# Kernel tuning notes

Hardware: AMD Instinct MI355X
Metric: run time of the kernel (lower is better)

Reference implementation:

```python
import jax, jax.numpy as jnp
import numpy as np

D_MODEL, D_FF, N_EXPERTS, TOP_K = 1024, 4096, 8, 2


def setup_inputs() -> dict:
    key = jax.random.key(0)
    k1, k2, k3, k4 = jax.random.split(key, 4)
    x = jax.random.normal(k1, (2, 2048, D_MODEL), dtype=jnp.float32)
    Wg = jax.random.normal(k2, (D_MODEL, N_EXPERTS), dtype=jnp.float32) * 0.02
    W1 = jax.random.normal(k3, (N_EXPERTS, D_MODEL, D_FF), dtype=jnp.float32) * 0.02
    b1 = jnp.zeros((N_EXPERTS, D_FF), dtype=jnp.float32)
    W2 = jax.random.normal(k4, (N_EXPERTS, D_FF, D_MODEL), dtype=jnp.float32) * 0.02
    b2 = jnp.zeros((N_EXPERTS, D_MODEL), dtype=jnp.float32)
    return {"x": x, "Wg": Wg, "W1": W1, "b1": b1, "W2": W2, "b2": b2}


def reference(x, Wg, W1, b1, W2, b2):
    B, S, D = x.shape
    T = B * S
    flat_x = x.reshape(T, D)                      # [T, D]
    # Router: softmax over expert logits, keep top-k experts per token.
    logits = flat_x @ Wg                          # [T, E]
    probs = jax.nn.softmax(logits, axis=-1)       # [T, E]
    _, top_idx = jax.lax.top_k(probs, TOP_K)      # [T, K]
    # mask[t, e] = 1 if expert e is among token t's top-k
    mask = jax.nn.one_hot(top_idx, N_EXPERTS, dtype=probs.dtype).sum(axis=1)  # [T, E]
    weights = probs * mask                        # gating score only for routed experts
    # Dense grouped expert MLP: every expert applied to all tokens, then masked-combined.
    h = jax.nn.gelu(jnp.einsum('td,edh->eth', flat_x, W1) + b1[:, None, :])  # [E, T, H]
    y = jnp.einsum('eth,ehd->etd', h, W2) + b2[:, None, :]                   # [E, T, D]
    out = jnp.einsum('etd,te->td', y, weights)                               # [T, D]
    return out.reshape(B, S, D)
```

## Files before the change

kernel.cpp:

```cpp
#include <hip/hip_runtime.h>
#include <hip/hip_bf16.h>

#define D_MODEL 1024
#define D_FF    4096
#define N_EXPERTS 8
#define TOPK    2
#define T_TOK   4096
#define NPAIR   (T_TOK * TOPK)
#define MT_MAX  32

typedef __attribute__((ext_vector_type(8))) short s8v;
typedef __attribute__((ext_vector_type(4))) float f4v;
typedef __attribute__((ext_vector_type(8))) unsigned short u16x8;

__device__ __forceinline__ void async16(const void* g, void* l) {
    __builtin_amdgcn_global_load_lds(
        (const __attribute__((address_space(1))) void*)g,
        (__attribute__((address_space(3))) void*)l, 16, 0, 0);
}

__device__ __forceinline__ float gelu_tanh(float v) {
    float u = 0.7978845608028654f * (v + 0.044715f * v * v * v);
    float t = 1.0f - 2.0f / (1.0f + __expf(2.0f * u));
    return 0.5f * v * (1.0f + t);
}

__device__ __forceinline__ unsigned short f2bf(float f) {
    union { __hip_bfloat16 b; unsigned short u; } cv;
    cv.b = __float2bfloat16(f);
    return cv.u;
}

__global__ __launch_bounds__(256) void router_kernel(
    const float* __restrict__ x, const float* __restrict__ Wg,
    int* __restrict__ top_e, float* __restrict__ top_w,
    int* __restrict__ counts)
{
    int wave = threadIdx.x >> 6;
    int lane = threadIdx.x & 63;
    int t = blockIdx.x * 4 + wave;
    if (t >= T_TOK) return;

    float acc[8] = {0.f,0.f,0.f,0.f,0.f,0.f,0.f,0.f};
    const float* xr = x + (size_t)t * D_MODEL;
    for (int d = lane; d < D_MODEL; d += 64) {
        float xv = xr[d];
        const float* wr = Wg + d * N_EXPERTS;
        float4 w0 = *(const float4*)wr;
        float4 w1 = *(const float4*)(wr + 4);
        acc[0] += xv * w0.x; acc[1] += xv * w0.y;
        acc[2] += xv * w0.z; acc[3] += xv * w0.w;
        acc[4] += xv * w1.x; acc[5] += xv * w1.y;
        acc[6] += xv * w1.z; acc[7] += xv * w1.w;
    }
    #pragma unroll
    for (int off = 32; off >= 1; off >>= 1) {
        #pragma unroll
        for (int e = 0; e < 8; e++) acc[e] += __shfl_xor(acc[e], off);
    }
    if (lane == 0) {
        float m = acc[0];
        #pragma unroll
        for (int e = 1; e < 8; e++) m = fmaxf(m, acc[e]);
        float p[8]; float s = 0.f;
        #pragma unroll
        for (int e = 0; e < 8; e++) { p[e] = expf(acc[e] - m); s += p[e]; }
        float inv = 1.f / s;
        #pragma unroll
        for (int e = 0; e < 8; e++) p[e] *= inv;
        int i0 = 0; float b0 = p[0];
        #pragma unroll
        for (int e = 1; e < 8; e++) if (p[e] > b0) { b0 = p[e]; i0 = e; }
        int i1 = -1; float b1 = -1.f;
        #pragma unroll
        for (int e = 0; e < 8; e++) if (e != i0 && p[e] > b1) { b1 = p[e]; i1 = e; }
        top_e[2*t]   = i0; top_w[2*t]   = b0;
        top_e[2*t+1] = i1; top_w[2*t+1] = b1;
        atomicAdd(&counts[i0], 1);
        atomicAdd(&counts[i1], 1);
    }
}

__global__ void offsets_kernel(const int* __restrict__ counts, int* __restrict__ offsets)
{
    if (threadIdx.x == 0 && blockIdx.x == 0) {
        int run = 0;
        for (int e = 0; e < N_EXPERTS; e++) { offsets[e] = run; run += counts[e]; }
        offsets[N_EXPERTS] = run;
    }
}

__global__ __launch_bounds__(256) void scatter_kernel(
    const int* __restrict__ top_e, const int* __restrict__ offsets,
    int* __restrict__ counts2, int* __restrict__ pair_id)
{
    int t = blockIdx.x * blockDim.x + threadIdx.x;
    if (t >= T_TOK) return;
    #pragma unroll
    for (int k = 0; k < TOPK; k++) {
        int e = top_e[2*t + k];
        int pos = atomicAdd(&counts2[e], 1);
        pair_id[offsets[e] + pos] = 2*t + k;
    }
}

__global__ __launch_bounds__(256) void cast_x_kernel(
    const float* __restrict__ x, __hip_bfloat16* __restrict__ xb)
{
    int i = (blockIdx.x * 256 + threadIdx.x) * 8;
    float4 a = *(const float4*)(x + i);
    float4 b = *(const float4*)(x + i + 4);
    unsigned short t[8];
    t[0]=f2bf(a.x); t[1]=f2bf(a.y); t[2]=f2bf(a.z); t[3]=f2bf(a.w);
    t[4]=f2bf(b.x); t[5]=f2bf(b.y); t[6]=f2bf(b.z); t[7]=f2bf(b.w);
    *(u16x8*)((unsigned short*)xb + i) = *(u16x8*)t;
}

__global__ __launch_bounds__(256) void transpose_cast_kernel(
    const float* __restrict__ src, __hip_bfloat16* __restrict__ dst, int R, int C)
{
    int e = blockIdx.z;
    src += (size_t)e * R * C;
    dst += (size_t)e * R * C;
    int b0 = blockIdx.x * 64;
    int a0 = blockIdx.y * 64;

    __shared__ float tile[64][65];
    int tid = threadIdx.x;
    int lr = tid >> 4;
    int lc = (tid & 15) * 4;
    #pragma unroll
    for (int rr = 0; rr < 4; rr++) {
        int r = lr + rr * 16;
        *(float4*)&tile[r][lc] = *(const float4*)(src + (size_t)(a0 + r) * C + b0 + lc);
    }
    __syncthreads();
    int oc = tid >> 3;
    int oj = (tid & 7) * 8;
    #pragma unroll
    for (int rr = 0; rr < 2; rr++) {
        int c = oc + rr * 32;
        unsigned short t[8];
        #pragma unroll
        for (int j = 0; j < 8; j++) t[j] = f2bf(tile[oj + j][c]);
        *(u16x8*)((unsigned short*)dst + (size_t)(b0 + c) * R + a0 + oj) = *(u16x8*)t;
    }
}

__global__ __launch_bounds__(256) void gemm1_mfma(
    const __hip_bfloat16* __restrict__ xb, const __hip_bfloat16* __restrict__ W1T,
    const float* __restrict__ b1,
    const int* __restrict__ offsets, const int* __restrict__ pair_id,
    __hip_bfloat16* __restrict__ h)
{
    int e  = blockIdx.y >> 5;
    int mt = blockIdx.y & 31;
    int off_e = offsets[e];
    int cnt   = offsets[e + 1] - off_e;
    int m0 = mt * 128;
    if (m0 >= cnt) return;
    int n0 = blockIdx.x * 128;

    __shared__ __hip_bfloat16 As[128 * 32];
    __shared__ __hip_bfloat16 Bs[128 * 32];
    __shared__ int pid[128];

    int tid = threadIdx.x;
    if (tid < 128) {
        int r = m0 + tid; if (r >= cnt) r = cnt - 1;
        pid[tid] = pair_id[off_e + r];
    }
    __syncthreads();

    int lane = tid & 63, wid = tid >> 6;
    int ia0 = wid * 64 + lane;
    int ia1 = ia0 + 256;
    int rA0 = ia0 >> 2, kA0 = (ia0 & 3) * 8;
    int rA1 = ia1 >> 2, kA1 = (ia1 & 3) * 8;

    const __hip_bfloat16* gA0 = xb + (size_t)(pid[rA0] >> 1) * D_MODEL + kA0;
    const __hip_bfloat16* gA1 = xb + (size_t)(pid[rA1] >> 1) * D_MODEL + kA1;
    const __hip_bfloat16* WT  = W1T + (size_t)e * (D_MODEL * D_FF);
    const __hip_bfloat16* gB0 = WT + (size_t)(n0 + rA0) * D_MODEL + kA0;
    const __hip_bfloat16* gB1 = WT + (size_t)(n0 + rA1) * D_MODEL + kA1;

    int fm = lane & 15;
    int fk = (lane >> 4) * 8;
    int wm = (wid >> 1) * 64;
    int wn = (wid & 1) * 64;

    f4v acc[4][4];
    #pragma unroll
    for (int i = 0; i < 4; i++)
        #pragma unroll
        for (int j = 0; j < 4; j++)
            acc[i][j] = (f4v){0.f, 0.f, 0.f, 0.f};

    for (int k0 = 0; k0 < D_MODEL; k0 += 32) {
        async16(gA0 + k0, As + ia0 * 8);
        async16(gA1 + k0, As + ia1 * 8);
        async16(gB0 + k0, Bs + ia0 * 8);
        async16(gB1 + k0, Bs + ia1 * 8);
        __syncthreads();
        s8v af[4], bfr[4];
        #pragma unroll
        for (int i = 0; i < 4; i++)
            af[i] = *(const s8v*)(As + (wm + i * 16 + fm) * 32 + fk);
        #pragma unroll
        for (int j = 0; j < 4; j++)
            bfr[j] = *(const s8v*)(Bs + (wn + j * 16 + fm) * 32 + fk);
        #pragma unroll
        for (int i = 0; i < 4; i++)
            #pragma unroll
            for (int j = 0; j < 4; j++)
                acc[i][j] = __builtin_amdgcn_mfma_f32_16x16x32_bf16(af[i], bfr[j], acc[i][j], 0, 0, 0);
        __syncthreads();
    }

    int rq = (lane >> 4) * 4;
    #pragma unroll
    for (int i = 0; i < 4; i++) {
        #pragma unroll
        for (int j = 0; j < 4; j++) {
            int n = n0 + wn + j * 16 + fm;
            float bias = b1[e * D_FF + n];
            #pragma unroll
            for (int r = 0; r < 4; r++) {
                int m = wm + i * 16 + rq + r;
                if (m0 + m < cnt) {
                    float v = acc[i][j][r] + bias;
                    h[(size_t)(off_e + m0 + m) * D_FF + n] = __float2bfloat16(gelu_tanh(v));
                }
            }
        }
    }
}

__global__ __launch_bounds__(256) void gemm2_mfma(
    const __hip_bfloat16* __restrict__ h, const __hip_bfloat16* __restrict__ W2T,
    const float* __restrict__ b2,
    const int* __restrict__ offsets, const int* __restrict__ pair_id,
    float* __restrict__ y)
{
    int e  = blockIdx.y >> 5;
    int mt = blockIdx.y & 31;
    int off_e = offsets[e];
    int cnt   = offsets[e + 1] - off_e;
    int m0 = mt * 128;
    if (m0 >= cnt) return;
    int n0 = blockIdx.x * 128;

    __shared__ __hip_bfloat16 As[128 * 32];
    __shared__ __hip_bfloat16 Bs[128 * 32];
    __shared__ int pid[128];

    int tid = threadIdx.x;
    if (tid < 128) {
        int r = m0 + tid; if (r >= cnt) r = cnt - 1;
        pid[tid] = pair_id[off_e + r];
    }
    __syncthreads();

    int lane = tid & 63, wid = tid >> 6;
    int ia0 = wid * 64 + lane;
    int ia1 = ia0 + 256;
    int rA0 = ia0 >> 2, kA0 = (ia0 & 3) * 8;
    int rA1 = ia1 >> 2, kA1 = (ia1 & 3) * 8;
    int mr0 = m0 + rA0; if (mr0 >= cnt) mr0 = cnt - 1;
    int mr1 = m0 + rA1; if (mr1 >= cnt) mr1 = cnt - 1;

    const __hip_bfloat16* gA0 = h + (size_t)(off_e + mr0) * D_FF + kA0;
    const __hip_bfloat16* gA1 = h + (size_t)(off_e + mr1) * D_FF + kA1;
    const __hip_bfloat16* WT  = W2T + (size_t)e * (D_FF * D_MODEL);
    const __hip_bfloat16* gB0 = WT + (size_t)(n0 + rA0) * D_FF + kA0;
    const __hip_bfloat16* gB1 = WT + (size_t)(n0 + rA1) * D_FF + kA1;

    int fm = lane & 15;
    int fk = (lane >> 4) * 8;
    int wm = (wid >> 1) * 64;
    int wn = (wid & 1) * 64;

    f4v acc[4][4];
    #pragma unroll
    for (int i = 0; i < 4; i++)
        #pragma unroll
        for (int j = 0; j < 4; j++)
            acc[i][j] = (f4v){0.f, 0.f, 0.f, 0.f};

    for (int k0 = 0; k0 < D_FF; k0 += 32) {
        async16(gA0 + k0, As + ia0 * 8);
        async16(gA1 + k0, As + ia1 * 8);
        async16(gB0 + k0, Bs + ia0 * 8);
        async16(gB1 + k0, Bs + ia1 * 8);
        __syncthreads();
        s8v af[4], bfr[4];
        #pragma unroll
        for (int i = 0; i < 4; i++)
            af[i] = *(const s8v*)(As + (wm + i * 16 + fm) * 32 + fk);
        #pragma unroll
        for (int j = 0; j < 4; j++)
            bfr[j] = *(const s8v*)(Bs + (wn + j * 16 + fm) * 32 + fk);
        #pragma unroll
        for (int i = 0; i < 4; i++)
            #pragma unroll
            for (int j = 0; j < 4; j++)
                acc[i][j] = __builtin_amdgcn_mfma_f32_16x16x32_bf16(af[i], bfr[j], acc[i][j], 0, 0, 0);
        __syncthreads();
    }

    int rq = (lane >> 4) * 4;
    #pragma unroll
    for (int i = 0; i < 4; i++) {
        #pragma unroll
        for (int j = 0; j < 4; j++) {
            int n = n0 + wn + j * 16 + fm;
            float bias = b2[e * D_MODEL + n];
            #pragma unroll
            for (int r = 0; r < 4; r++) {
                int m = wm + i * 16 + rq + r;
                if (m0 + m < cnt) {
                    int p = pid[m];
                    y[(size_t)p * D_MODEL + n] = acc[i][j][r] + bias;
                }
            }
        }
    }
}

__global__ __launch_bounds__(256) void combine_kernel(
    const float* __restrict__ y, const float* __restrict__ top_w,
    float* __restrict__ out)
{
    int gid = blockIdx.x * blockDim.x + threadIdx.x;
    int t = gid >> 8;
    int c = gid & 255;
    float w0 = top_w[2*t];
    float w1 = top_w[2*t + 1];
    const float4* y0 = (const float4*)(y + (size_t)(2*t) * D_MODEL);
    const float4* y1 = (const float4*)(y + (size_t)(2*t + 1) * D_MODEL);
    float4 a = y0[c], b = y1[c];
    float4 o;
    o.x = w0*a.x + w1*b.x; o.y = w0*a.y + w1*b.y;
    o.z = w0*a.z + w1*b.z; o.w = w0*a.w + w1*b.w;
    ((float4*)out)[gid] = o;
}

extern "C" void kernel_launch(void* const* d_in, const int* in_sizes, int n_in,
                              void* d_out, int out_size, void* d_ws, size_t ws_size,
                              hipStream_t stream)
{
    const float* x  = (const float*)d_in[0];
    const float* Wg = (const float*)d_in[1];
    const float* W1 = (const float*)d_in[2];
    const float* b1 = (const float*)d_in[3];
    const float* W2 = (const float*)d_in[4];
    const float* b2 = (const float*)d_in[5];
    float* out = (float*)d_out;

    char* ws = (char*)d_ws;
    size_t off = 0;
    int*   top_e   = (int*)(ws + off);  off += (size_t)NPAIR * 4;
    float* top_w   = (float*)(ws + off); off += (size_t)NPAIR * 4;
    int*   counts  = (int*)(ws + off);
    int*   counts2 = counts + N_EXPERTS;
    int*   offsets = counts2 + N_EXPERTS; off += 256;
    int*   pair_id = (int*)(ws + off);  off += (size_t)NPAIR * 4;
    off = (off + 255) & ~(size_t)255;
    __hip_bfloat16* xb  = (__hip_bfloat16*)(ws + off); off += (size_t)T_TOK * D_MODEL * 2;
    __hip_bfloat16* W1T = (__hip_bfloat16*)(ws + off); off += (size_t)N_EXPERTS * D_MODEL * D_FF * 2;
    __hip_bfloat16* W2T = (__hip_bfloat16*)(ws + off); off += (size_t)N_EXPERTS * D_MODEL * D_FF * 2;
    __hip_bfloat16* h   = (__hip_bfloat16*)(ws + off); off += (size_t)NPAIR * D_FF * 2;
    float*          y   = (float*)(ws + off);          off += (size_t)NPAIR * D_MODEL * 4;

    hipMemsetAsync(counts, 0, 256, stream);

    router_kernel<<<T_TOK / 4, 256, 0, stream>>>(x, Wg, top_e, top_w, counts);
    offsets_kernel<<<1, 64, 0, stream>>>(counts, offsets);
    scatter_kernel<<<T_TOK / 256, 256, 0, stream>>>(top_e, offsets, counts2, pair_id);

    cast_x_kernel<<<(T_TOK * D_MODEL) / (256 * 8), 256, 0, stream>>>(x, xb);
    transpose_cast_kernel<<<dim3(D_FF / 64, D_MODEL / 64, N_EXPERTS), 256, 0, stream>>>(
        W1, W1T, D_MODEL, D_FF);
    transpose_cast_kernel<<<dim3(D_MODEL / 64, D_FF / 64, N_EXPERTS), 256, 0, stream>>>(
        W2, W2T, D_FF, D_MODEL);

    gemm1_mfma<<<dim3(D_FF / 128, N_EXPERTS * MT_MAX), 256, 0, stream>>>(
        xb, W1T, b1, offsets, pair_id, h);
    gemm2_mfma<<<dim3(D_MODEL / 128, N_EXPERTS * MT_MAX), 256, 0, stream>>>(
        h, W2T, b2, offsets, pair_id, y);
    combine_kernel<<<T_TOK, 256, 0, stream>>>(y, top_w, out);
}
```

Baseline: 737.3 us.

## Split-K the second expert GEMM and swizzle LDS tile layout for fragment reads

gemm2 now splits the D_FF reduction into two halves, doubling the number of blocks. Each half writes its own partial output buffer, and the combine kernel sums the partials before applying the gate weights. Both GEMMs also remap the async global-to-LDS copy so that each 16-row by 8-k fragment is stored contiguously, which lets each lane read its MFMA operand with a lane*8 offset and should reduce LDS bank conflicts. The split-K adds an extra fp32 partial buffer of NPAIR x D_MODEL, so combine reads twice as much data.

```diff
diff --git a/kernel.cpp b/kernel.cpp
--- a/kernel.cpp
+++ b/kernel.cpp
@@ -8,6 +8,7 @@
 #define T_TOK   4096
 #define NPAIR   (T_TOK * TOPK)
 #define MT_MAX  32
+#define KSPLIT  2
 
 typedef __attribute__((ext_vector_type(8))) short s8v;
 typedef __attribute__((ext_vector_type(4))) float f4v;
@@ -173,21 +174,21 @@
     __syncthreads();
 
     int lane = tid & 63, wid = tid >> 6;
-    int ia0 = wid * 64 + lane;
-    int ia1 = ia0 + 256;
-    int rA0 = ia0 >> 2, kA0 = (ia0 & 3) * 8;
-    int rA1 = ia1 >> 2, kA1 = (ia1 & 3) * 8;
-
-    const __hip_bfloat16* gA0 = xb + (size_t)(pid[rA0] >> 1) * D_MODEL + kA0;
-    const __hip_bfloat16* gA1 = xb + (size_t)(pid[rA1] >> 1) * D_MODEL + kA1;
+    int c0 = tid, c1 = tid + 256;
+    int r0 = ((c0 >> 6) << 4) | (c0 & 15), kb0 = (c0 >> 4) & 3;
+    int r1 = ((c1 >> 6) << 4) | (c1 & 15), kb1 = (c1 >> 4) & 3;
+
+    const __hip_bfloat16* gA0 = xb + (size_t)(pid[r0] >> 1) * D_MODEL + kb0 * 8;
+    const __hip_bfloat16* gA1 = xb + (size_t)(pid[r1] >> 1) * D_MODEL + kb1 * 8;
     const __hip_bfloat16* WT  = W1T + (size_t)e * (D_MODEL * D_FF);
-    const __hip_bfloat16* gB0 = WT + (size_t)(n0 + rA0) * D_MODEL + kA0;
-    const __hip_bfloat16* gB1 = WT + (size_t)(n0 + rA1) * D_MODEL + kA1;
+    const __hip_bfloat16* gB0 = WT + (size_t)(n0 + r0) * D_MODEL + kb0 * 8;
+    const __hip_bfloat16* gB1 = WT + (size_t)(n0 + r1) * D_MODEL + kb1 * 8;
 
     int fm = lane & 15;
-    int fk = (lane >> 4) * 8;
     int wm = (wid >> 1) * 64;
     int wn = (wid & 1) * 64;
+    int rba = (wid >> 1) * 4;
+    int rbb = (wid & 1) * 4;
 
     f4v acc[4][4];
     #pragma unroll
@@ -197,18 +198,18 @@
             acc[i][j] = (f4v){0.f, 0.f, 0.f, 0.f};
 
     for (int k0 = 0; k0 < D_MODEL; k0 += 32) {
-        async16(gA0 + k0, As + ia0 * 8);
-        async16(gA1 + k0, As + ia1 * 8);
-        async16(gB0 + k0, Bs + ia0 * 8);
-        async16(gB1 + k0, Bs + ia1 * 8);
+        async16(gA0 + k0, As + c0 * 8);
+        async16(gA1 + k0, As + c1 * 8);
+        async16(gB0 + k0, Bs + c0 * 8);
+        async16(gB1 + k0, Bs + c1 * 8);
         __syncthreads();
         s8v af[4], bfr[4];
         #pragma unroll
         for (int i = 0; i < 4; i++)
-            af[i] = *(const s8v*)(As + (wm + i * 16 + fm) * 32 + fk);
+            af[i] = *(const s8v*)(As + (rba + i) * 512 + lane * 8);
         #pragma unroll
         for (int j = 0; j < 4; j++)
-            bfr[j] = *(const s8v*)(Bs + (wn + j * 16 + fm) * 32 + fk);
+            bfr[j] = *(const s8v*)(Bs + (rbb + j) * 512 + lane * 8);
         #pragma unroll
         for (int i = 0; i < 4; i++)
             #pragma unroll
@@ -240,15 +241,19 @@
     const __hip_bfloat16* __restrict__ h, const __hip_bfloat16* __restrict__ W2T,
     const float* __restrict__ b2,
     const int* __restrict__ offsets, const int* __restrict__ pair_id,
-    float* __restrict__ y)
-{
-    int e  = blockIdx.y >> 5;
-    int mt = blockIdx.y & 31;
+    float* __restrict__ yp)
+{
+    int bz = blockIdx.y;
+    int s  = bz & (KSPLIT - 1);
+    int mt = (bz / KSPLIT) & 31;
+    int e  = bz / (KSPLIT * 32);
     int off_e = offsets[e];
     int cnt   = offsets[e + 1] - off_e;
     int m0 = mt * 128;
     if (m0 >= cnt) return;
     int n0 = blockIdx.x * 128;
+    int kbeg = s * (D_FF / KSPLIT);
+    int kend = kbeg + D_FF / KSPLIT;
 
     __shared__ __hip_bfloat16 As[128 * 32];
     __shared__ __hip_bfloat16 Bs[128 * 32];
@@ -262,23 +267,23 @@
     __syncthreads();
 
     int lane = tid & 63, wid = tid >> 6;
-    int ia0 = wid * 64 + lane;
-    int ia1 = ia0 + 256;
-    int rA0 = ia0 >> 2, kA0 = (ia0 & 3) * 8;
-    int rA1 = ia1 >> 2, kA1 = (ia1 & 3) * 8;
-    int mr0 = m0 + rA0; if (mr0 >= cnt) mr0 = cnt - 1;
-    int mr1 = m0 + rA1; if (mr1 >= cnt) mr1 = cnt - 1;
-
-    const __hip_bfloat16* gA0 = h + (size_t)(off_e + mr0) * D_FF + kA0;
-    const __hip_bfloat16* gA1 = h + (size_t)(off_e + mr1) * D_FF + kA1;
+    int c0 = tid, c1 = tid + 256;
+    int r0 = ((c0 >> 6) << 4) | (c0 & 15), kb0 = (c0 >> 4) & 3;
+    int r1 = ((c1 >> 6) << 4) | (c1 & 15), kb1 = (c1 >> 4) & 3;
+    int mr0 = m0 + r0; if (mr0 >= cnt) mr0 = cnt - 1;
+    int mr1 = m0 + r1; if (mr1 >= cnt) mr1 = cnt - 1;
+
+    const __hip_bfloat16* gA0 = h + (size_t)(off_e + mr0) * D_FF + kb0 * 8;
+    const __hip_bfloat16* gA1 = h + (size_t)(off_e + mr1) * D_FF + kb1 * 8;
     const __hip_bfloat16* WT  = W2T + (size_t)e * (D_FF * D_MODEL);
-    const __hip_bfloat16* gB0 = WT + (size_t)(n0 + rA0) * D_FF + kA0;
-    const __hip_bfloat16* gB1 = WT + (size_t)(n0 + rA1) * D_FF + kA1;
+    const __hip_bfloat16* gB0 = WT + (size_t)(n0 + r0) * D_FF + kb0 * 8;
+    const __hip_bfloat16* gB1 = WT + (size_t)(n0 + r1) * D_FF + kb1 * 8;
 
     int fm = lane & 15;
-    int fk = (lane >> 4) * 8;
     int wm = (wid >> 1) * 64;
     int wn = (wid & 1) * 64;
+    int rba = (wid >> 1) * 4;
+    int rbb = (wid & 1) * 4;
 
     f4v acc[4][4];
     #pragma unroll
@@ -287,19 +292,19 @@
         for (int j = 0; j < 4; j++)
             acc[i][j] = (f4v){0.f, 0.f, 0.f, 0.f};
 
-    for (int k0 = 0; k0 < D_FF; k0 += 32) {
-        async16(gA0 + k0, As + ia0 * 8);
-        async16(gA1 + k0, As + ia1 * 8);
-        async16(gB0 + k0, Bs + ia0 * 8);
-        async16(gB1 + k0, Bs + ia1 * 8);
+    for (int k0 = kbeg; k0 < kend; k0 += 32) {
+        async16(gA0 + k0, As + c0 * 8);
+        async16(gA1 + k0, As + c1 * 8);
+        async16(gB0 + k0, Bs + c0 * 8);
+        async16(gB1 + k0, Bs + c1 * 8);
         __syncthreads();
         s8v af[4], bfr[4];
         #pragma unroll
         for (int i = 0; i < 4; i++)
-            af[i] = *(const s8v*)(As + (wm + i * 16 + fm) * 32 + fk);
+            af[i] = *(const s8v*)(As + (rba + i) * 512 + lane * 8);
         #pragma unroll
         for (int j = 0; j < 4; j++)
-            bfr[j] = *(const s8v*)(Bs + (wn + j * 16 + fm) * 32 + fk);
+            bfr[j] = *(const s8v*)(Bs + (rbb + j) * 512 + lane * 8);
         #pragma unroll
         for (int i = 0; i < 4; i++)
             #pragma unroll
@@ -308,19 +313,20 @@
         __syncthreads();
     }
 
+    float* yout = yp + (size_t)s * NPAIR * D_MODEL;
     int rq = (lane >> 4) * 4;
     #pragma unroll
     for (int i = 0; i < 4; i++) {
         #pragma unroll
         for (int j = 0; j < 4; j++) {
             int n = n0 + wn + j * 16 + fm;
-            float bias = b2[e * D_MODEL + n];
+            float bias = (s == 0) ? b2[e * D_MODEL + n] : 0.f;
             #pragma unroll
             for (int r = 0; r < 4; r++) {
                 int m = wm + i * 16 + rq + r;
                 if (m0 + m < cnt) {
                     int p = pid[m];
-                    y[(size_t)p * D_MODEL + n] = acc[i][j][r] + bias;
+                    yout[(size_t)p * D_MODEL + n] = acc[i][j][r] + bias;
                 }
             }
         }
@@ -328,7 +334,7 @@
 }
 
 __global__ __launch_bounds__(256) void combine_kernel(
-    const float* __restrict__ y, const float* __restrict__ top_w,
+    const float* __restrict__ yp, const float* __restrict__ top_w,
     float* __restrict__ out)
 {
     int gid = blockIdx.x * blockDim.x + threadIdx.x;
@@ -336,12 +342,17 @@
     int c = gid & 255;
     float w0 = top_w[2*t];
     float w1 = top_w[2*t + 1];
-    const float4* y0 = (const float4*)(y + (size_t)(2*t) * D_MODEL);
-    const float4* y1 = (const float4*)(y + (size_t)(2*t + 1) * D_MODEL);
-    float4 a = y0[c], b = y1[c];
+    const float4* y0a = (const float4*)(yp + (size_t)(2*t) * D_MODEL);
+    const float4* y1a = (const float4*)(yp + (size_t)(2*t + 1) * D_MODEL);
+    const float4* y0b = (const float4*)(yp + (size_t)NPAIR * D_MODEL + (size_t)(2*t) * D_MODEL);
+    const float4* y1b = (const float4*)(yp + (size_t)NPAIR * D_MODEL + (size_t)(2*t + 1) * D_MODEL);
+    float4 a0 = y0a[c], a1 = y0b[c];
+    float4 b0 = y1a[c], b1 = y1b[c];
     float4 o;
-    o.x = w0*a.x + w1*b.x; o.y = w0*a.y + w1*b.y;
-    o.z = w0*a.z + w1*b.z; o.w = w0*a.w + w1*b.w;
+    o.x = w0*(a0.x+a1.x) + w1*(b0.x+b1.x);
+    o.y = w0*(a0.y+a1.y) + w1*(b0.y+b1.y);
+    o.z = w0*(a0.z+a1.z) + w1*(b0.z+b1.z);
+    o.w = w0*(a0.w+a1.w) + w1*(b0.w+b1.w);
     ((float4*)out)[gid] = o;
 }
 
@@ -370,7 +381,7 @@
     __hip_bfloat16* W1T = (__hip_bfloat16*)(ws + off); off += (size_t)N_EXPERTS * D_MODEL * D_FF * 2;
     __hip_bfloat16* W2T = (__hip_bfloat16*)(ws + off); off += (size_t)N_EXPERTS * D_MODEL * D_FF * 2;
     __hip_bfloat16* h   = (__hip_bfloat16*)(ws + off); off += (size_t)NPAIR * D_FF * 2;
-    float*          y   = (float*)(ws + off);          off += (size_t)NPAIR * D_MODEL * 4;
+    float*          yp  = (float*)(ws + off);          off += (size_t)KSPLIT * NPAIR * D_MODEL * 4;
 
     hipMemsetAsync(counts, 0, 256, stream);
 
@@ -386,7 +397,7 @@
 
     gemm1_mfma<<<dim3(D_FF / 128, N_EXPERTS * MT_MAX), 256, 0, stream>>>(
         xb, W1T, b1, offsets, pair_id, h);
-    gemm2_mfma<<<dim3(D_MODEL / 128, N_EXPERTS * MT_MAX), 256, 0, stream>>>(
-        h, W2T, b2, offsets, pair_id, y);
-    combine_kernel<<<T_TOK, 256, 0, stream>>>(y, top_w, out);
-}
+    gemm2_mfma<<<dim3(D_MODEL / 128, N_EXPERTS * MT_MAX * KSPLIT), 256, 0, stream>>>(
+        h, W2T, b2, offsets, pair_id, yp);
+    combine_kernel<<<T_TOK, 256, 0, stream>>>(yp, top_w, out);
+}
```

Measured after the change: 848.1 us. 1.15x slower.
